# Kernel optimization log

Hardware: AMD Instinct MI355X
Metric: run time of the kernel (lower is better)

Reference implementation:

```python
import jax, jax.numpy as jnp
import numpy as np

HEADS = 12
EPS = 1e-12  # torch F.normalize eps


def _l2_normalize(x, axis):
    norm = jnp.sqrt(jnp.sum(x * x, axis=axis, keepdims=True))
    return x / jnp.maximum(norm, EPS)


def setup_inputs() -> dict:
    key = jax.random.key(0)
    k1, k2, k3 = jax.random.split(key, 3)
    B, N, D = 8, 4096, 768
    x = jax.random.normal(k1, (B, N, D), dtype=jnp.float32)
    Wqkv = jax.random.normal(k2, (D, 3 * D), dtype=jnp.float32) * (1.0 / np.sqrt(D))
    temperature = jnp.ones((1, HEADS, 1, 1), dtype=jnp.float32)
    Wout = jax.random.normal(k3, (D, D), dtype=jnp.float32) * (1.0 / np.sqrt(D))
    bout = jnp.zeros((D,), dtype=jnp.float32)
    return {"x": x, "Wqkv": Wqkv, "temperature": temperature, "Wout": Wout, "bout": bout}


def reference(x, Wqkv, temperature, Wout, bout):
    B, N, D = x.shape
    H = HEADS
    d = D // H
    qkv = x @ Wqkv  # (B, N, 3D)
    q, k, v = jnp.split(qkv, 3, axis=-1)
    # b n (h d) -> b h n d
    def to_bhnd(t):
        return t.reshape(B, N, H, d).transpose(0, 2, 1, 3)
    q = to_bhnd(q)
    k = to_bhnd(k)
    v = to_bhnd(v)
    # q: normalize over token axis (torch: q is bhnd, dim=-2 -> n)
    q = _l2_normalize(q, axis=2)
    # k: torch layout is bhdn, normalized over dim=-1 (n); in bhnd that's axis=2
    k = _l2_normalize(k, axis=2) * temperature  # (1,H,1,1) broadcasts over bhnd
    # attention[p, q_idx] = sum_n k[n, p] * q[n, q_idx]  -> (B, H, d, d)
    attn = jnp.einsum('bhnp,bhnq->bhpq', k, q)
    attn = jax.nn.softmax(attn, axis=-1)
    # out[n, q_idx] = sum_p v[n, p] * attn[p, q_idx]
    out = jnp.einsum('bhnp,bhpq->bhnq', v, attn)
    # b h n d -> b n (h d)
    out = out.transpose(0, 2, 1, 3).reshape(B, N, D)
    return out @ Wout + bout
```

## Files before the change

### kernel.cpp

```cpp
#include <hip/hip_runtime.h>

typedef __attribute__((ext_vector_type(8))) short short8;
typedef __attribute__((ext_vector_type(4))) float f32x4;

__device__ __forceinline__ float b2f(unsigned short u) {
    unsigned int i = ((unsigned int)u) << 16;
    return __builtin_bit_cast(float, i);
}
__device__ __forceinline__ unsigned short f2b(float f) {
    unsigned int u = __builtin_bit_cast(unsigned int, f);
    unsigned int r = (u + 0x7fffu + ((u >> 16) & 1u)) >> 16;
    return (unsigned short)r;
}

__device__ __forceinline__ void async16(unsigned short* lds, const unsigned short* g) {
    __builtin_amdgcn_global_load_lds(
        (const __attribute__((address_space(1))) unsigned int*)g,
        (__attribute__((address_space(3))) unsigned int*)lds,
        16, 0, 0);
}

__device__ __forceinline__ void xcd_swizzle(int& bx, int& by) {
    if ((gridDim.y & 7) == 0) {
        const int nx = gridDim.x;
        const int rows_per_xcd = gridDim.y >> 3;
        const int flat = blockIdx.y * nx + blockIdx.x;
        const int xcd = flat & 7;
        const int i = flat >> 3;
        by = xcd * rows_per_xcd + i / nx;
        bx = i % nx;
    } else {
        bx = blockIdx.x; by = blockIdx.y;
    }
}

__global__ __launch_bounds__(256)
void wprep(const float* __restrict__ in, unsigned short* __restrict__ outT,
           unsigned short* __restrict__ rm, int R, int C) {
    __shared__ unsigned short t[32][33];
    const int r0 = blockIdx.y * 32, c0 = blockIdx.x * 32;
    const int tx = threadIdx.x & 31, ty = threadIdx.x >> 5;
    #pragma unroll
    for (int i = 0; i < 32; i += 8) {
        unsigned short v = f2b(in[(size_t)(r0 + ty + i) * C + c0 + tx]);
        t[ty + i][tx] = v;
        if (rm) rm[(size_t)(r0 + ty + i) * C + c0 + tx] = v;
    }
    __syncthreads();
    #pragma unroll
    for (int i = 0; i < 32; i += 8)
        outT[(size_t)(c0 + ty + i) * R + r0 + tx] = t[tx][ty + i];
}

__global__ __launch_bounds__(256)
void cvt_tr64(const float* __restrict__ in, unsigned short* __restrict__ rm,
              unsigned short* __restrict__ tm) {
    __shared__ unsigned short T[64][72];
    const int c0 = blockIdx.x * 64, r0 = blockIdx.y * 64;
    const int tr = threadIdx.x >> 2, tc = (threadIdx.x & 3) * 16;
    {
        const float* src = in + (size_t)(r0 + tr) * 768 + c0 + tc;
        f32x4 a0 = *(const f32x4*)(src);
        f32x4 a1 = *(const f32x4*)(src + 4);
        f32x4 a2 = *(const f32x4*)(src + 8);
        f32x4 a3 = *(const f32x4*)(src + 12);
        short8 o0, o1;
        #pragma unroll
        for (int j = 0; j < 4; ++j) {
            o0[j] = (short)f2b(a0[j]); o0[j + 4] = (short)f2b(a1[j]);
            o1[j] = (short)f2b(a2[j]); o1[j + 4] = (short)f2b(a3[j]);
        }
        *(short8*)&T[tr][tc] = o0;
        *(short8*)&T[tr][tc + 8] = o1;
        unsigned short* d = rm + (size_t)(r0 + tr) * 768 + c0 + tc;
        *(short8*)(d) = o0;
        *(short8*)(d + 8) = o1;
    }
    __syncthreads();
    short8 s0, s1;
    #pragma unroll
    for (int e = 0; e < 8; ++e) {
        s0[e] = (short)T[tc + e][tr];
        s1[e] = (short)T[tc + 8 + e][tr];
    }
    unsigned short* d = tm + (size_t)(c0 + tr) * 32768 + r0 + tc;
    *(short8*)(d) = s0;
    *(short8*)(d + 8) = s1;
}

__device__ __forceinline__ void tri_rc(int t, int& r, int& c) {
    r = 0;
    int rem = t;
    while (rem >= 6 - r) { rem -= 6 - r; ++r; }
    c = r + rem;
}

__global__ __launch_bounds__(256, 4)
void gram_split_sym(const unsigned short* __restrict__ xT, unsigned short* __restrict__ Gp) {
    __shared__ unsigned short As[128 * 32];
    __shared__ unsigned short Bs[128 * 32];
    const int z = blockIdx.y, b = z >> 3, s = z & 7;
    int tr_, tc_;
    tri_rc(blockIdx.x, tr_, tc_);
    const int tid  = threadIdx.x;
    const int wave = tid >> 6, lane = tid & 63;
    const int quad = lane >> 4, m16 = lane & 15;
    const int bm = tr_ * 128, bn = tc_ * 128;
    const int wm = (wave >> 1) * 64, wn = (wave & 1) * 64;
    const int srow = wave * 32 + (lane >> 2);
    const int scol = (lane & 3) * 8;
    const unsigned short* base = xT + (size_t)b * 4096 + s * 512 + scol;
    const unsigned short* Ag = base + (size_t)(bm + srow) * 32768;
    const unsigned short* Bg = base + (size_t)(bn + srow) * 32768;
    unsigned short* Asw = &As[(wave * 32) * 32];
    unsigned short* Bsw = &Bs[(wave * 32) * 32];
    f32x4 acc[4][4] = {};

    for (int k0 = 0; k0 < 512; k0 += 32) {
        __syncthreads();
        async16(Asw,           Ag + k0);
        async16(Asw + 16 * 32, Ag + k0 + (size_t)16 * 32768);
        async16(Bsw,           Bg + k0);
        async16(Bsw + 16 * 32, Bg + k0 + (size_t)16 * 32768);
        __syncthreads();
        short8 af[4], bfr[4];
        #pragma unroll
        for (int i = 0; i < 4; ++i)
            af[i] = *(const short8*)&As[(wm + i * 16 + m16) * 32 + quad * 8];
        #pragma unroll
        for (int j = 0; j < 4; ++j)
            bfr[j] = *(const short8*)&Bs[(wn + j * 16 + m16) * 32 + quad * 8];
        #pragma unroll
        for (int i = 0; i < 4; ++i)
            #pragma unroll
            for (int j = 0; j < 4; ++j)
                acc[i][j] = __builtin_amdgcn_mfma_f32_16x16x32_bf16(af[i], bfr[j], acc[i][j], 0, 0, 0);
    }
    unsigned short* C = Gp + ((size_t)z * 21 + blockIdx.x) * 16384;
    #pragma unroll
    for (int j = 0; j < 4; ++j) {
        const int col = wn + j * 16 + m16;
        #pragma unroll
        for (int i = 0; i < 4; ++i)
            #pragma unroll
            for (int r = 0; r < 4; ++r) {
                const int row = wm + i * 16 + quad * 4 + r;
                C[row * 128 + col] = f2b(acc[i][j][r]);
            }
    }
}

__global__ __launch_bounds__(256)
void g_reduce_sym(const unsigned short* __restrict__ Gp, unsigned short* __restrict__ G) {
    const int t = blockIdx.x, b = blockIdx.y;
    int r, c;
    tri_rc(t, r, c);
    __shared__ unsigned short T[128][136];
    const int tid = threadIdx.x;
    const int row = tid >> 1, colbase = (tid & 1) * 64;
    unsigned short* Gb = G + (size_t)b * 589824;
    const unsigned short* p0 = Gp + ((size_t)(b * 8) * 21 + t) * 16384 + row * 128;
    #pragma unroll
    for (int k = 0; k < 8; ++k) {
        const int col = colbase + k * 8;
        float sum[8] = {};
        #pragma unroll
        for (int s = 0; s < 8; ++s) {
            short8 v = *(const short8*)(p0 + (size_t)s * 21 * 16384 + col);
            #pragma unroll
            for (int e = 0; e < 8; ++e) sum[e] += b2f((unsigned short)v[e]);
        }
        short8 o;
        #pragma unroll
        for (int e = 0; e < 8; ++e) o[e] = (short)f2b(sum[e]);
        *(short8*)&Gb[(size_t)(r * 128 + row) * 768 + c * 128 + col] = o;
        *(short8*)&T[row][col] = o;
    }
    if (r != c) {
        __syncthreads();
        #pragma unroll
        for (int k = 0; k < 8; ++k) {
            const int col = colbase + k * 8;
            short8 m;
            #pragma unroll
            for (int e = 0; e < 8; ++e) m[e] = (short)T[col + e][row];
            *(short8*)&Gb[(size_t)(c * 128 + row) * 768 + r * 128 + col] = m;
        }
    }
}

template<int OM>
__global__ __launch_bounds__(256, 4)
void gemm_bt_g(const unsigned short* A, const unsigned short* BT,
               void* __restrict__ Cv, const float* __restrict__ bias,
               int K, int lda, int ldb, int ldc,
               long long sA, long long sB, long long sC) {
    __shared__ unsigned short As[128 * 32];
    __shared__ unsigned short Bs[128 * 32];
    const int z = blockIdx.z;
    A  += (size_t)z * sA;
    BT += (size_t)z * sB;
    int bxi, byi;
    xcd_swizzle(bxi, byi);
    const int tid  = threadIdx.x;
    const int wave = tid >> 6, lane = tid & 63;
    const int quad = lane >> 4, m16 = lane & 15;
    const int bm = byi * 128, bn = bxi * 128;
    const int wm = (wave >> 1) * 64, wn = (wave & 1) * 64;
    const int srow = wave * 32 + (lane >> 2);
    const int scol = (lane & 3) * 8;
    const unsigned short* Ag = A + (size_t)(bm + srow) * lda + scol;
    const unsigned short* Bg = BT + (size_t)(bn + srow) * ldb + scol;
    unsigned short* Asw = &As[(wave * 32) * 32];
    unsigned short* Bsw = &Bs[(wave * 32) * 32];
    f32x4 acc[4][4] = {};

    for (int k0 = 0; k0 < K; k0 += 32) {
        __syncthreads();
        async16(Asw,           Ag + k0);
        async16(Asw + 16 * 32, Ag + k0 + (size_t)16 * lda);
        async16(Bsw,           Bg + k0);
        async16(Bsw + 16 * 32, Bg + k0 + (size_t)16 * ldb);
        __syncthreads();
        short8 af[4], bfr[4];
        #pragma unroll
        for (int i = 0; i < 4; ++i)
            af[i] = *(const short8*)&As[(wm + i * 16 + m16) * 32 + quad * 8];
        #pragma unroll
        for (int j = 0; j < 4; ++j)
            bfr[j] = *(const short8*)&Bs[(wn + j * 16 + m16) * 32 + quad * 8];
        #pragma unroll
        for (int i = 0; i < 4; ++i)
            #pragma unroll
            for (int j = 0; j < 4; ++j)
                acc[i][j] = __builtin_amdgcn_mfma_f32_16x16x32_bf16(af[i], bfr[j], acc[i][j], 0, 0, 0);
    }

    if constexpr (OM == 0) {
        unsigned short* C = (unsigned short*)Cv + (size_t)z * sC;
        #pragma unroll
        for (int j = 0; j < 4; ++j) {
            const int col = bn + wn + j * 16 + m16;
            #pragma unroll
            for (int i = 0; i < 4; ++i)
                #pragma unroll
                for (int r = 0; r < 4; ++r) {
                    const int row = bm + wm + i * 16 + quad * 4 + r;
                    C[(size_t)row * ldc + col] = f2b(acc[i][j][r]);
                }
        }
    } else {
        float* C = (float*)Cv + (size_t)z * sC;
        #pragma unroll
        for (int j = 0; j < 4; ++j) {
            const int col = bn + wn + j * 16 + m16;
            const float bv = bias[col];
            #pragma unroll
            for (int i = 0; i < 4; ++i)
                #pragma unroll
                for (int r = 0; r < 4; ++r) {
                    const int row = bm + wm + i * 16 + quad * 4 + r;
                    C[(size_t)row * ldc + col] = acc[i][j][r] + bv;
                }
        }
    }
}

__global__ __launch_bounds__(256)
void rownorm(const unsigned short* __restrict__ W, const unsigned short* __restrict__ T,
             float* __restrict__ qn2, float* __restrict__ kn2) {
    const int row = blockIdx.x * 4 + (threadIdx.x >> 6);
    const int lane = threadIdx.x & 63;
    const int b = row / 1536, j = row % 1536;
    const unsigned short* wr = W + (size_t)j * 768;
    const unsigned short* tr = T + (size_t)b * 1179648 + (size_t)j * 768;
    float s = 0.f;
    {
        short8 a = *(const short8*)(wr + lane * 8);
        short8 c = *(const short8*)(tr + lane * 8);
        #pragma unroll
        for (int e = 0; e < 8; ++e) s += b2f((unsigned short)a[e]) * b2f((unsigned short)c[e]);
    }
    if (lane < 32) {
        short8 a = *(const short8*)(wr + 512 + lane * 8);
        short8 c = *(const short8*)(tr + 512 + lane * 8);
        #pragma unroll
        for (int e = 0; e < 8; ++e) s += b2f((unsigned short)a[e]) * b2f((unsigned short)c[e]);
    }
    #pragma unroll
    for (int o = 32; o; o >>= 1) s += __shfl_down(s, o);
    if (lane == 0) {
        if (j < 768) qn2[b * 768 + j] = s;
        else         kn2[b * 768 + j - 768] = s;
    }
}

__global__ __launch_bounds__(256)
void head_fused(const unsigned short* __restrict__ WqkvT,
                const unsigned short* __restrict__ TQKT,
                const unsigned short* __restrict__ Wbf,
                const float* __restrict__ qn2, const float* __restrict__ kn2,
                const float* __restrict__ temp, unsigned short* __restrict__ W2) {
    const int bh = blockIdx.x, b = bh / 12, h = bh % 12;
    __shared__ unsigned short As[64][72], Bs[64][72], At[64][72];
    __shared__ float Sf[64][65];
    __shared__ float qinv[64], kinv[64], red[64][4], red2[64][4];
    const int tid = threadIdx.x;
    const int wave = tid >> 6, lane = tid & 63;
    const int quad = lane >> 4, m16 = lane & 15;
    const int wr = wave >> 1, wc = wave & 1;

    if (tid < 64) {
        qinv[tid] = 1.0f / fmaxf(sqrtf(qn2[b * 768 + h * 64 + tid]), 1e-12f);
        kinv[tid] = 1.0f / fmaxf(sqrtf(kn2[b * 768 + h * 64 + tid]), 1e-12f);
    }

    f32x4 sacc[2][2] = {};
    const int srow = tid >> 3, scol8 = (tid & 7) * 8;
    const unsigned short* Arow = WqkvT + (size_t)(768 + h * 64) * 768;
    const unsigned short* Brow = TQKT + (size_t)(b * 1536 + h * 64) * 768;
    for (int k0 = 0; k0 < 768; k0 += 64) {
        __syncthreads();
        *(short8*)&As[srow][scol8]      = *(const short8*)(Arow + (size_t)srow * 768 + k0 + scol8);
        *(short8*)&As[srow + 32][scol8] = *(const short8*)(Arow + (size_t)(srow + 32) * 768 + k0 + scol8);
        *(short8*)&Bs[srow][scol8]      = *(const short8*)(Brow + (size_t)srow * 768 + k0 + scol8);
        *(short8*)&Bs[srow + 32][scol8] = *(const short8*)(Brow + (size_t)(srow + 32) * 768 + k0 + scol8);
        __syncthreads();
        #pragma unroll
        for (int ks = 0; ks < 2; ++ks) {
            short8 af[2], bv[2];
            af[0] = *(const short8*)&As[wr * 32 + m16][ks * 32 + quad * 8];
            af[1] = *(const short8*)&As[wr * 32 + 16 + m16][ks * 32 + quad * 8];
            bv[0] = *(const short8*)&Bs[wc * 32 + m16][ks * 32 + quad * 8];
            bv[1] = *(const short8*)&Bs[wc * 32 + 16 + m16][ks * 32 + quad * 8];
            #pragma unroll
            for (int i = 0; i < 2; ++i)
                #pragma unroll
                for (int j = 0; j < 2; ++j)
                    sacc[i][j] = __builtin_amdgcn_mfma_f32_16x16x32_bf16(af[i], bv[j], sacc[i][j], 0, 0, 0);
        }
    }
    __syncthreads();
    #pragma unroll
    for (int i = 0; i < 2; ++i)
        #pragma unroll
        for (int j = 0; j < 2; ++j)
            #pragma unroll
            for (int r = 0; r < 4; ++r)
                Sf[wr * 32 + i * 16 + quad * 4 + r][wc * 32 + j * 16 + m16] = sacc[i][j][r];
    __syncthreads();

    const float tt = temp[h];
    const int p = tid & 63, g = tid >> 6;
    float l[16], mx = -1e30f;
    const float kvp = tt * kinv[p];
    #pragma unroll
    for (int e = 0; e < 16; ++e) {
        l[e] = kvp * Sf[p][g * 16 + e] * qinv[g * 16 + e];
        mx = fmaxf(mx, l[e]);
    }
    red[p][g] = mx;
    __syncthreads();
    mx = fmaxf(fmaxf(red[p][0], red[p][1]), fmaxf(red[p][2], red[p][3]));
    float sum = 0.f;
    #pragma unroll
    for (int e = 0; e < 16; ++e) { l[e] = __expf(l[e] - mx); sum += l[e]; }
    red2[p][g] = sum;
    __syncthreads();
    sum = red2[p][0] + red2[p][1] + red2[p][2] + red2[p][3];
    const float inv = 1.0f / sum;
    #pragma unroll
    for (int e = 0; e < 16; ++e) At[g * 16 + e][p] = f2b(l[e] * inv);
    __syncthreads();

    const unsigned short* Wv = Wbf + 1536 + h * 64;
    unsigned short* W2b = W2 + (size_t)b * 589824 + h * 64;
    #pragma unroll
    for (int pass = 0; pass < 3; ++pass) {
        const int rb = wave * 192 + pass * 64;
        f32x4 wacc[4][4] = {};
        #pragma unroll
        for (int ks = 0; ks < 2; ++ks) {
            short8 av[4], bv[4];
            #pragma unroll
            for (int i = 0; i < 4; ++i)
                av[i] = *(const short8*)(Wv + (size_t)(rb + i * 16 + m16) * 2304 + ks * 32 + quad * 8);
            #pragma unroll
            for (int j = 0; j < 4; ++j)
                bv[j] = *(const short8*)&At[j * 16 + m16][ks * 32 + quad * 8];
            #pragma unroll
            for (int i = 0; i < 4; ++i)
                #pragma unroll
                for (int j = 0; j < 4; ++j)
                    wacc[i][j] = __builtin_amdgcn_mfma_f32_16x16x32_bf16(av[i], bv[j], wacc[i][j], 0, 0, 0);
        }
        #pragma unroll
        for (int j = 0; j < 4; ++j)
            #pragma unroll
            for (int i = 0; i < 4; ++i)
                #pragma unroll
                for (int r = 0; r < 4; ++r)
                    W2b[(size_t)(rb + i * 16 + quad * 4 + r) * 768 + j * 16 + m16] = f2b(wacc[i][j][r]);
    }
}

extern "C" void kernel_launch(void* const* d_in, const int* in_sizes, int n_in,
                              void* d_out, int out_size, void* d_ws, size_t ws_size,
                              hipStream_t stream) {
    const float *x = nullptr, *Wqkv = nullptr, *temp = nullptr, *Wout = nullptr, *bout = nullptr;
    for (int i = 0; i < n_in; ++i) {
        switch (in_sizes[i]) {
            case 25165824: x    = (const float*)d_in[i]; break;
            case 1769472:  Wqkv = (const float*)d_in[i]; break;
            case 12:       temp = (const float*)d_in[i]; break;
            case 589824:   Wout = (const float*)d_in[i]; break;
            case 768:      bout = (const float*)d_in[i]; break;
        }
    }
    float* out = (float*)d_out;

    char* ws = (char*)d_ws;
    unsigned short* WqkvT = (unsigned short*)(ws + 0);
    unsigned short* WoutT = (unsigned short*)(ws + 3538944);
    unsigned short* Wbf   = (unsigned short*)(ws + 4718592);
    unsigned short* xb    = (unsigned short*)(ws + 8257536);
    unsigned short* xT    = (unsigned short*)(ws + 58589184);
    unsigned short* G     = (unsigned short*)(ws + 58589184);
    unsigned short* TQKT  = (unsigned short*)(ws + 68026368);
    float*          qn2   = (float*)         (ws + 86900736);
    float*          kn2   = (float*)         (ws + 86925312);
    unsigned short* W2    = (unsigned short*)(ws + 86949888);
    unsigned short* FT    = (unsigned short*)(ws + 96387072);
    unsigned short* Gp    = (unsigned short*)(ws + 108920832);
    (void)ws_size;

    wprep<<<dim3(72, 24), 256, 0, stream>>>(Wqkv, WqkvT, Wbf, 768, 2304);
    wprep<<<dim3(24, 24), 256, 0, stream>>>(Wout, WoutT, nullptr, 768, 768);

    cvt_tr64<<<dim3(12, 512), 256, 0, stream>>>(x, xb, xT);

    gram_split_sym<<<dim3(21, 64), 256, 0, stream>>>(xT, Gp);
    g_reduce_sym<<<dim3(21, 8), 256, 0, stream>>>(Gp, G);

    gemm_bt_g<0><<<dim3(6, 12, 8), 256, 0, stream>>>(
        WqkvT, G, TQKT, nullptr, 768, 768, 768, 768, 0LL, 589824LL, 1179648LL);

    rownorm<<<dim3(3072), 256, 0, stream>>>(WqkvT, TQKT, qn2, kn2);

    head_fused<<<dim3(96), 256, 0, stream>>>(WqkvT, TQKT, Wbf, qn2, kn2, temp, W2);

    gemm_bt_g<0><<<dim3(6, 6, 8), 256, 0, stream>>>(
        WoutT, W2, FT, nullptr, 768, 768, 768, 768, 0LL, 589824LL, 589824LL);

    gemm_bt_g<2><<<dim3(6, 32, 8), 256, 0, stream>>>(
        xb, FT, out, bout, 768, 768, 768, 768, 3145728LL, 589824LL, 3145728LL);
}
```

Before: 438.4 us.

## Use BK=64 XOR-swizzled LDS tiles for gram and final GEMM, split head_fused

The Gram kernel now uses 64-wide K tiles with an XOR-swizzled LDS layout, and it splits K into 4 chunks instead of 8. That halves the partial buffers the reduce step has to sum. A new gemm_bt64 kernel with the same swizzled 64-wide tiling replaces the final output GEMM. head_fused now spreads its three output passes across a second grid dimension, which recomputes the softmax per block in exchange for more parallelism. The larger LDS footprint lowers the occupancy hint from 4 to 2 blocks.

```diff
diff --git a/kernel.cpp b/kernel.cpp
--- a/kernel.cpp
+++ b/kernel.cpp
@@ -95,11 +95,12 @@
     c = r + rem;
 }
 
-__global__ __launch_bounds__(256, 4)
-void gram_split_sym(const unsigned short* __restrict__ xT, unsigned short* __restrict__ Gp) {
-    __shared__ unsigned short As[128 * 32];
-    __shared__ unsigned short Bs[128 * 32];
-    const int z = blockIdx.y, b = z >> 3, s = z & 7;
+
+__global__ __launch_bounds__(256, 2)
+void gram64_sym(const unsigned short* __restrict__ xT, unsigned short* __restrict__ Gp) {
+    __shared__ unsigned short As[128 * 64];
+    __shared__ unsigned short Bs[128 * 64];
+    const int z = blockIdx.y, b = z >> 2, s = z & 3;
     int tr_, tc_;
     tri_rc(blockIdx.x, tr_, tc_);
     const int tid  = threadIdx.x;
@@ -107,34 +108,42 @@
     const int quad = lane >> 4, m16 = lane & 15;
     const int bm = tr_ * 128, bn = tc_ * 128;
     const int wm = (wave >> 1) * 64, wn = (wave & 1) * 64;
-    const int srow = wave * 32 + (lane >> 2);
-    const int scol = (lane & 3) * 8;
-    const unsigned short* base = xT + (size_t)b * 4096 + s * 512 + scol;
+    const int srow = tid >> 3;
+    const int sc = ((tid & 7) ^ (srow & 7)) * 8;
+    const unsigned short* base = xT + (size_t)b * 4096 + s * 1024 + sc;
     const unsigned short* Ag = base + (size_t)(bm + srow) * 32768;
     const unsigned short* Bg = base + (size_t)(bn + srow) * 32768;
-    unsigned short* Asw = &As[(wave * 32) * 32];
-    unsigned short* Bsw = &Bs[(wave * 32) * 32];
+    unsigned short* Asl = As + wave * 512;
+    unsigned short* Bsl = Bs + wave * 512;
     f32x4 acc[4][4] = {};
 
-    for (int k0 = 0; k0 < 512; k0 += 32) {
-        __syncthreads();
-        async16(Asw,           Ag + k0);
-        async16(Asw + 16 * 32, Ag + k0 + (size_t)16 * 32768);
-        async16(Bsw,           Bg + k0);
-        async16(Bsw + 16 * 32, Bg + k0 + (size_t)16 * 32768);
-        __syncthreads();
-        short8 af[4], bfr[4];
-        #pragma unroll
-        for (int i = 0; i < 4; ++i)
-            af[i] = *(const short8*)&As[(wm + i * 16 + m16) * 32 + quad * 8];
-        #pragma unroll
-        for (int j = 0; j < 4; ++j)
-            bfr[j] = *(const short8*)&Bs[(wn + j * 16 + m16) * 32 + quad * 8];
-        #pragma unroll
-        for (int i = 0; i < 4; ++i)
-            #pragma unroll
-            for (int j = 0; j < 4; ++j)
-                acc[i][j] = __builtin_amdgcn_mfma_f32_16x16x32_bf16(af[i], bfr[j], acc[i][j], 0, 0, 0);
+    for (int k0 = 0; k0 < 1024; k0 += 64) {
+        __syncthreads();
+        #pragma unroll
+        for (int is = 0; is < 4; ++is) {
+            async16(Asl + is * 2048, Ag + k0 + (size_t)(is * 32) * 32768);
+            async16(Bsl + is * 2048, Bg + k0 + (size_t)(is * 32) * 32768);
+        }
+        __syncthreads();
+        #pragma unroll
+        for (int ks = 0; ks < 2; ++ks) {
+            short8 af[4], bfr[4];
+            #pragma unroll
+            for (int i = 0; i < 4; ++i) {
+                const int r = wm + i * 16 + m16;
+                af[i] = *(const short8*)&As[r * 64 + (((ks * 4 + quad) ^ (r & 7)) << 3)];
+            }
+            #pragma unroll
+            for (int j = 0; j < 4; ++j) {
+                const int r = wn + j * 16 + m16;
+                bfr[j] = *(const short8*)&Bs[r * 64 + (((ks * 4 + quad) ^ (r & 7)) << 3)];
+            }
+            #pragma unroll
+            for (int i = 0; i < 4; ++i)
+                #pragma unroll
+                for (int j = 0; j < 4; ++j)
+                    acc[i][j] = __builtin_amdgcn_mfma_f32_16x16x32_bf16(af[i], bfr[j], acc[i][j], 0, 0, 0);
+        }
     }
     unsigned short* C = Gp + ((size_t)z * 21 + blockIdx.x) * 16384;
     #pragma unroll
@@ -159,13 +168,13 @@
     const int tid = threadIdx.x;
     const int row = tid >> 1, colbase = (tid & 1) * 64;
     unsigned short* Gb = G + (size_t)b * 589824;
-    const unsigned short* p0 = Gp + ((size_t)(b * 8) * 21 + t) * 16384 + row * 128;
+    const unsigned short* p0 = Gp + ((size_t)(b * 4) * 21 + t) * 16384 + row * 128;
     #pragma unroll
     for (int k = 0; k < 8; ++k) {
         const int col = colbase + k * 8;
         float sum[8] = {};
         #pragma unroll
-        for (int s = 0; s < 8; ++s) {
+        for (int s = 0; s < 4; ++s) {
             short8 v = *(const short8*)(p0 + (size_t)s * 21 * 16384 + col);
             #pragma unroll
             for (int e = 0; e < 8; ++e) sum[e] += b2f((unsigned short)v[e]);
@@ -185,6 +194,91 @@
             #pragma unroll
             for (int e = 0; e < 8; ++e) m[e] = (short)T[col + e][row];
             *(short8*)&Gb[(size_t)(c * 128 + row) * 768 + r * 128 + col] = m;
+        }
+    }
+}
+
+template<int OM>
+__global__ __launch_bounds__(256, 2)
+void gemm_bt64(const unsigned short* A, const unsigned short* BT,
+               void* __restrict__ Cv, const float* __restrict__ bias,
+               int K, int lda, int ldb, int ldc,
+               long long sA, long long sB, long long sC) {
+    __shared__ unsigned short As[128 * 64];
+    __shared__ unsigned short Bs[128 * 64];
+    const int z = blockIdx.z;
+    A  += (size_t)z * sA;
+    BT += (size_t)z * sB;
+    int bxi, byi;
+    xcd_swizzle(bxi, byi);
+    const int tid  = threadIdx.x;
+    const int wave = tid >> 6, lane = tid & 63;
+    const int quad = lane >> 4, m16 = lane & 15;
+    const int bm = byi * 128, bn = bxi * 128;
+    const int wm = (wave >> 1) * 64, wn = (wave & 1) * 64;
+    const int srow = tid >> 3;
+    const int sc = ((tid & 7) ^ (srow & 7)) * 8;
+    const unsigned short* Ag = A + (size_t)(bm + srow) * lda + sc;
+    const unsigned short* Bg = BT + (size_t)(bn + srow) * ldb + sc;
+    unsigned short* Asl = As + wave * 512;
+    unsigned short* Bsl = Bs + wave * 512;
+    f32x4 acc[4][4] = {};
+
+    for (int k0 = 0; k0 < K; k0 += 64) {
+        __syncthreads();
+        #pragma unroll
+        for (int is = 0; is < 4; ++is) {
+            async16(Asl + is * 2048, Ag + k0 + (size_t)(is * 32) * lda);
+            async16(Bsl + is * 2048, Bg + k0 + (size_t)(is * 32) * ldb);
+        }
+        __syncthreads();
+        #pragma unroll
+        for (int ks = 0; ks < 2; ++ks) {
+            short8 af[4], bfr[4];
+            #pragma unroll
+            for (int i = 0; i < 4; ++i) {
+                const int r = wm + i * 16 + m16;
+                af[i] = *(const short8*)&As[r * 64 + (((ks * 4 + quad) ^ (r & 7)) << 3)];
+            }
+            #pragma unroll
+            for (int j = 0; j < 4; ++j) {
+                const int r = wn + j * 16 + m16;
+                bfr[j] = *(const short8*)&Bs[r * 64 + (((ks * 4 + quad) ^ (r & 7)) << 3)];
+            }
+            #pragma unroll
+            for (int i = 0; i < 4; ++i)
+                #pragma unroll
+                for (int j = 0; j < 4; ++j)
+                    acc[i][j] = __builtin_amdgcn_mfma_f32_16x16x32_bf16(af[i], bfr[j], acc[i][j], 0, 0, 0);
+        }
+    }
+
+    if constexpr (OM == 0) {
+        unsigned short* C = (unsigned short*)Cv + (size_t)z * sC;
+        #pragma unroll
+        for (int j = 0; j < 4; ++j) {
+            const int col = bn + wn + j * 16 + m16;
+            #pragma unroll
+            for (int i = 0; i < 4; ++i)
+                #pragma unroll
+                for (int r = 0; r < 4; ++r) {
+                    const int row = bm + wm + i * 16 + quad * 4 + r;
+                    C[(size_t)row * ldc + col] = f2b(acc[i][j][r]);
+                }
+        }
+    } else {
+        float* C = (float*)Cv + (size_t)z * sC;
+        #pragma unroll
+        for (int j = 0; j < 4; ++j) {
+            const int col = bn + wn + j * 16 + m16;
+            const float bv = bias[col];
+            #pragma unroll
+            for (int i = 0; i < 4; ++i)
+                #pragma unroll
+                for (int r = 0; r < 4; ++r) {
+                    const int row = bm + wm + i * 16 + quad * 4 + r;
+                    C[(size_t)row * ldc + col] = acc[i][j][r] + bv;
+                }
         }
     }
 }
@@ -373,10 +467,10 @@
     for (int e = 0; e < 16; ++e) At[g * 16 + e][p] = f2b(l[e] * inv);
     __syncthreads();
 
+    const int pass = blockIdx.y;
     const unsigned short* Wv = Wbf + 1536 + h * 64;
     unsigned short* W2b = W2 + (size_t)b * 589824 + h * 64;
-    #pragma unroll
-    for (int pass = 0; pass < 3; ++pass) {
+    {
         const int rb = wave * 192 + pass * 64;
         f32x4 wacc[4][4] = {};
         #pragma unroll
@@ -439,7 +533,7 @@
 
     cvt_tr64<<<dim3(12, 512), 256, 0, stream>>>(x, xb, xT);
 
-    gram_split_sym<<<dim3(21, 64), 256, 0, stream>>>(xT, Gp);
+    gram64_sym<<<dim3(21, 32), 256, 0, stream>>>(xT, Gp);
     g_reduce_sym<<<dim3(21, 8), 256, 0, stream>>>(Gp, G);
 
     gemm_bt_g<0><<<dim3(6, 12, 8), 256, 0, stream>>>(
@@ -447,11 +541,11 @@
 
     rownorm<<<dim3(3072), 256, 0, stream>>>(WqkvT, TQKT, qn2, kn2);
 
-    head_fused<<<dim3(96), 256, 0, stream>>>(WqkvT, TQKT, Wbf, qn2, kn2, temp, W2);
+    head_fused<<<dim3(96, 3), 256, 0, stream>>>(WqkvT, TQKT, Wbf, qn2, kn2, temp, W2);
 
     gemm_bt_g<0><<<dim3(6, 6, 8), 256, 0, stream>>>(
         WoutT, W2, FT, nullptr, 768, 768, 768, 768, 0LL, 589824LL, 589824LL);
 
-    gemm_bt_g<2><<<dim3(6, 32, 8), 256, 0, stream>>>(
+    gemm_bt64<2><<<dim3(6, 32, 8), 256, 0, stream>>>(
         xb, FT, out, bout, 768, 768, 768, 768, 3145728LL, 589824LL, 3145728LL);
 }
```

Measured after the change: 393.4 us. -10.3%, faster.
